# Kernel tuning notes

Measured on AMD Instinct MI355X. Metric: run time of the kernel, lower is better.

The kernel has to match this reference:

```python
import jax, jax.numpy as jnp
import numpy as np

H = 8          # num_heads
D = 64         # head_dim
IN = 512       # input_dim
SCALE = D ** -0.5


def setup_inputs() -> dict:
    key = jax.random.key(0)
    ks = jax.random.split(key, 5)
    b, n = 4, 2048
    inner = H * D
    x = jax.random.normal(ks[0], (b, n, IN), dtype=jnp.float32)
    # nn.Linear weights stored as [out, in]; apply as x @ W.T
    Wq = jax.random.normal(ks[1], (inner, IN), dtype=jnp.float32) * (IN ** -0.5)
    Wkv = jax.random.normal(ks[2], (2 * inner, IN), dtype=jnp.float32) * (IN ** -0.5)
    Wo = jax.random.normal(ks[3], (IN, inner), dtype=jnp.float32) * (inner ** -0.5)
    bo = jax.random.normal(ks[4], (IN,), dtype=jnp.float32) * 0.01
    return {"x": x, "Wq": Wq, "Wkv": Wkv, "Wo": Wo, "bo": bo}


def reference(x, Wq, Wkv, Wo, bo):
    b, n, _ = x.shape
    q = jnp.einsum('bni,oi->bno', x, Wq).reshape(b, n, H, D).transpose(0, 2, 1, 3)
    kv = jnp.einsum('bni,oi->bno', x, Wkv)
    k, v = jnp.split(kv, 2, axis=-1)
    k = k.reshape(b, n, H, D).transpose(0, 2, 1, 3)
    v = v.reshape(b, n, H, D).transpose(0, 2, 1, 3)
    attn = jax.nn.softmax(jnp.einsum('bhnd,bhmd->bhnm', q, k) * SCALE, axis=-1)
    # dropout in eval mode: identity
    out = jnp.einsum('bhnm,bhmd->bhnd', attn, v)
    out = out.transpose(0, 2, 1, 3).reshape(b, n, H * D)
    return jnp.einsum('bno,io->bni', out, Wo) + bo
```

## Files before the change

### kernel.cpp

```cpp
#include <hip/hip_runtime.h>
#include <hip/hip_bf16.h>

#define H_ 8
#define D_ 64
#define IN_ 512
#define B_ 4
#define N_ 2048
#define TOK_ (B_*N_)
#define CLOG2_ 0.18033688011112042f

typedef __attribute__((ext_vector_type(8))) short short8;
typedef __attribute__((ext_vector_type(4))) short bs4;
typedef __attribute__((ext_vector_type(4))) float f32x4;

__device__ __forceinline__ unsigned short f2bf(float f) {
  unsigned int u = __float_as_uint(f);
  u += 0x7FFFu + ((u >> 16) & 1u);
  return (unsigned short)(u >> 16);
}

__device__ __forceinline__ short8 cvt8(const float4 a, const float4 b) {
  union { short8 v; __hip_bfloat162 h[4]; } z;
  z.h[0] = __float22bfloat162_rn(make_float2(a.x, a.y));
  z.h[1] = __float22bfloat162_rn(make_float2(a.z, a.w));
  z.h[2] = __float22bfloat162_rn(make_float2(b.x, b.y));
  z.h[3] = __float22bfloat162_rn(make_float2(b.z, b.w));
  return z.v;
}

__device__ __forceinline__ bs4 pack4(float a, float b, float c, float d) {
  union { bs4 v; __hip_bfloat162 h[2]; } z;
  z.h[0] = __float22bfloat162_rn(make_float2(a, b));
  z.h[1] = __float22bfloat162_rn(make_float2(c, d));
  return z.v;
}

__device__ __forceinline__ short8 assemble_p(bs4 pa, bs4 pb) {
  union { bs4 v; unsigned int w[2]; } A, B;
  A.v = pa; B.v = pb;
  auto s0 = __builtin_amdgcn_permlane32_swap(A.w[0], B.w[0], false, false);
  auto s1 = __builtin_amdgcn_permlane32_swap(A.w[1], B.w[1], false, false);
  auto t0 = __builtin_amdgcn_permlane16_swap(s0[0], s0[1], false, false);
  auto t1 = __builtin_amdgcn_permlane16_swap(s1[0], s1[1], false, false);
  union { short8 v; unsigned int w[4]; } R;
  R.w[0] = t0[0];
  R.w[1] = t1[0];
  R.w[2] = t0[1];
  R.w[3] = t1[1];
  return R.v;
}

__device__ __forceinline__ void gld16(const unsigned short* g, unsigned short* l) {
  __builtin_amdgcn_global_load_lds(
      (const __attribute__((address_space(1))) void*)g,
      (__attribute__((address_space(3))) void*)l, 16, 0, 0);
}

__global__ __launch_bounds__(256) void conv_all_kernel(
    const float* __restrict__ x, const float* __restrict__ Wq,
    const float* __restrict__ Wkv, const float* __restrict__ Wo,
    unsigned short* __restrict__ xbf, unsigned short* __restrict__ wbf,
    unsigned short* __restrict__ wobf)
{
  const int b = blockIdx.x;
  const float* src;
  unsigned short* dst;
  size_t base;
  if (b < 2048)      { src = x;   dst = xbf;             base = (size_t)b * 2048; }
  else if (b < 2176) { src = Wq;  dst = wbf;             base = (size_t)(b - 2048) * 2048; }
  else if (b < 2432) { src = Wkv; dst = wbf + 512 * 512; base = (size_t)(b - 2176) * 2048; }
  else               { src = Wo;  dst = wobf;            base = (size_t)(b - 2432) * 2048; }
  size_t i = base + (size_t)threadIdx.x * 8;
  float4 a = *(const float4*)(src + i);
  float4 c = *(const float4*)(src + i + 4);
  *(short8*)(dst + i) = cvt8(a, c);
}

__global__ __launch_bounds__(256) void qkv_gemm_kernel(
    const unsigned short* __restrict__ xbf, const unsigned short* __restrict__ wbf,
    unsigned short* __restrict__ qws, unsigned short* __restrict__ kws,
    unsigned short* __restrict__ vws)
{
  __shared__ __attribute__((aligned(16))) unsigned short sm[128 * 136];

  const int lid = blockIdx.x + (blockIdx.y << 6);
  const int swz = (lid & 7) * 96 + (lid >> 3);
  const int t0 = (swz / 12) * 128;
  const int c0 = (swz % 12) * 128;
  const int cls = c0 >> 9;

  const int tid = threadIdx.x;
  const int wave = tid >> 6, lane = tid & 63;
  const int quad = lane >> 4, l16 = lane & 15;
  const int wm = wave >> 1, wn = wave & 1;

  const int r_ = tid >> 2;
  const int gc = (tid & 3) ^ (r_ & 3);
  const unsigned short* abase = xbf + (size_t)(t0 + r_) * IN_ + gc * 8;
  const unsigned short* bbase = wbf + (size_t)(c0 + r_) * IN_ + gc * 8;

  auto stage = [&](int k0, int buf) {
    unsigned short* sA = sm + buf * 8192;
    unsigned short* sB = sA + 4096;
    gld16(abase + k0,            sA + tid * 8);
    gld16(abase + 64 * IN_ + k0, sA + 2048 + tid * 8);
    gld16(bbase + k0,            sB + tid * 8);
    gld16(bbase + 64 * IN_ + k0, sB + 2048 + tid * 8);
  };

  f32x4 acc[4][4];
  #pragma unroll
  for (int i = 0; i < 4; i++)
    #pragma unroll
    for (int j = 0; j < 4; j++) acc[i][j] = (f32x4){0.f, 0.f, 0.f, 0.f};

  stage(0, 0);

  for (int kt = 0; kt < 16; kt++) {
    const int cur = kt & 1;
    __syncthreads();
    if (kt + 1 < 16) stage((kt + 1) * 32, cur ^ 1);
    const unsigned short* sA = sm + cur * 8192;
    const unsigned short* sB = sA + 4096;
    const int sw = ((quad ^ (l16 & 3)) << 3);
    short8 af[4], bf[4];
    #pragma unroll
    for (int mi = 0; mi < 4; mi++)
      af[mi] = *(const short8*)&sA[(wm * 64 + mi * 16 + l16) * 32 + sw];
    #pragma unroll
    for (int ni = 0; ni < 4; ni++)
      bf[ni] = *(const short8*)&sB[(wn * 64 + ni * 16 + l16) * 32 + sw];
    #pragma unroll
    for (int mi = 0; mi < 4; mi++)
      #pragma unroll
      for (int ni = 0; ni < 4; ni++)
        acc[mi][ni] = __builtin_amdgcn_mfma_f32_16x16x32_bf16(af[mi], bf[ni], acc[mi][ni], 0, 0, 0);
  }

  __syncthreads();

  if (cls < 2) {
    const float qs = (cls == 0) ? CLOG2_ : 1.0f;
    #pragma unroll
    for (int mi = 0; mi < 4; mi++) {
      const int row0 = wm * 64 + mi * 16 + quad * 4;
      #pragma unroll
      for (int ni = 0; ni < 4; ni++) {
        const int col = wn * 64 + ni * 16 + l16;
        #pragma unroll
        for (int r = 0; r < 4; r++)
          sm[(row0 + r) * 136 + col] = f2bf(acc[mi][ni][r] * qs);
      }
    }
    __syncthreads();
    const int row = tid >> 1, half = tid & 1;
    const int t = t0 + row, bb = t >> 11, nn = t & (N_ - 1);
    const int cw = (c0 & 511) + half * 64;
    const int hh = cw >> 6;
    unsigned short* dst = ((cls == 0) ? qws : kws) +
                          ((size_t)(bb * H_ + hh) * N_ + nn) * D_;
    const unsigned short* srcp = &sm[row * 136 + half * 64];
    #pragma unroll
    for (int j = 0; j < 8; j++)
      *(uint4*)(dst + j * 8) = *(const uint4*)(srcp + j * 8);
  } else {
    #pragma unroll
    for (int mi = 0; mi < 4; mi++) {
      const int tk = wm * 64 + mi * 16 + quad * 4;
      #pragma unroll
      for (int ni = 0; ni < 4; ni++) {
        const int col = wn * 64 + ni * 16 + l16;
        bs4 pk4 = pack4(acc[mi][ni][0], acc[mi][ni][1], acc[mi][ni][2], acc[mi][ni][3]);
        *(bs4*)&sm[col * 136 + tk] = pk4;
      }
    }
    __syncthreads();
    const int col = tid >> 1, half = tid & 1;
    const int cw = (c0 - 1024) + col;
    const int hh = cw >> 6, dd = cw & 63;
    const int bb = t0 >> 11, n0 = (t0 & (N_ - 1)) + half * 64;
    unsigned short* dst = vws + ((size_t)(bb * H_ + hh) * D_ + dd) * N_ + n0;
    const unsigned short* srcp = &sm[col * 136 + half * 64];
    #pragma unroll
    for (int j = 0; j < 8; j++)
      *(uint4*)(dst + j * 8) = *(const uint4*)(srcp + j * 8);
  }
}

__global__ __launch_bounds__(512, 4) void attention_kernel(
    const unsigned short* __restrict__ qws,
    const unsigned short* __restrict__ kws,
    const unsigned short* __restrict__ vws,
    unsigned short* __restrict__ ows)
{
  __shared__ __attribute__((aligned(16))) unsigned short sm[2][8192];
  __shared__ float sml[128];

  const int lid = blockIdx.x + (blockIdx.y << 4);
  const int swz = ((lid & 7) << 6) + (lid >> 3);
  const int q0 = (swz & 15) * 128;
  const int bh = swz >> 4;
  const int tid = threadIdx.x;
  const int wave = tid >> 6, lane = tid & 63;
  const int quad = lane >> 4, l16 = lane & 15;
  const int rbw = wave & 3;
  const int kh = wave >> 2;

  const unsigned short* qbase = qws + (size_t)bh * N_ * D_;
  const unsigned short* kbase = kws + (size_t)bh * N_ * D_;
  const unsigned short* vbase = vws + (size_t)bh * D_ * N_;

  short8 qf[2][2];
  #pragma unroll
  for (int rb = 0; rb < 2; rb++) {
    const int qrow = q0 + rbw * 32 + rb * 16 + l16;
    #pragma unroll
    for (int kc = 0; kc < 2; kc++)
      qf[rb][kc] = *(const short8*)(qbase + (size_t)qrow * D_ + kc * 32 + quad * 8);
  }

  f32x4 ot[2][4];
  f32x4 otl[2];
  #pragma unroll
  for (int rb = 0; rb < 2; rb++) {
    #pragma unroll
    for (int db = 0; db < 4; db++) ot[rb][db] = (f32x4){0.f, 0.f, 0.f, 0.f};
    otl[rb] = (f32x4){0.f, 0.f, 0.f, 0.f};
  }
  const short8 ones8 = {(short)0x3F80, (short)0x3F80, (short)0x3F80, (short)0x3F80,
                        (short)0x3F80, (short)0x3F80, (short)0x3F80, (short)0x3F80};

  const int r_ = tid >> 3;
  const int gc = (tid & 7) ^ (r_ & 7);
  const unsigned short* kst = kbase + (size_t)r_ * D_ + gc * 8;
  const unsigned short* vst = vbase + (size_t)r_ * N_ + gc * 8;

  {
    gld16(kst, &sm[0][0]    + tid * 8);
    gld16(vst, &sm[0][4096] + tid * 8);
  }

  for (int kt = 0; kt < N_ / 64; kt++) {
    const int cur = kt & 1;
    __syncthreads();
    if (kt + 1 < N_ / 64) {
      const int k0 = (kt + 1) * 64;
      gld16(kst + (size_t)k0 * D_, &sm[cur ^ 1][0]    + tid * 8);
      gld16(vst + k0,              &sm[cur ^ 1][4096] + tid * 8);
    }
    const unsigned short* Ks = &sm[cur][0];
    const unsigned short* Vs = &sm[cur][4096];

    f32x4 st[2][2];
    #pragma unroll
    for (int rb = 0; rb < 2; rb++)
      #pragma unroll
      for (int nb = 0; nb < 2; nb++) st[rb][nb] = (f32x4){0.f, 0.f, 0.f, 0.f};
    #pragma unroll
    for (int kc = 0; kc < 2; kc++) {
      const int sw = (((kc * 4 + quad) ^ (l16 & 7)) << 3);
      #pragma unroll
      for (int nb = 0; nb < 2; nb++) {
        short8 kf = *(const short8*)&Ks[(kh * 32 + nb * 16 + l16) * 64 + sw];
        st[0][nb] = __builtin_amdgcn_mfma_f32_16x16x32_bf16(kf, qf[0][kc], st[0][nb], 0, 0, 0);
        st[1][nb] = __builtin_amdgcn_mfma_f32_16x16x32_bf16(kf, qf[1][kc], st[1][nb], 0, 0, 0);
      }
    }

    short8 pA[2];
    #pragma unroll
    for (int rb = 0; rb < 2; rb++) {
      bs4 pf[2];
      #pragma unroll
      for (int nb = 0; nb < 2; nb++) {
        float p0 = __builtin_amdgcn_exp2f(st[rb][nb][0]);
        float p1 = __builtin_amdgcn_exp2f(st[rb][nb][1]);
        float p2 = __builtin_amdgcn_exp2f(st[rb][nb][2]);
        float p3 = __builtin_amdgcn_exp2f(st[rb][nb][3]);
        pf[nb] = pack4(p0, p1, p2, p3);
      }
      pA[rb] = assemble_p(pf[0], pf[1]);
    }

    {
      const int slot = (((kh * 4 + quad) ^ (l16 & 7)) << 3);
      short8 vf8[4];
      #pragma unroll
      for (int db = 0; db < 4; db++)
        vf8[db] = *(const short8*)&Vs[(db * 16 + l16) * 64 + slot];
      #pragma unroll
      for (int rb = 0; rb < 2; rb++) {
        #pragma unroll
        for (int db = 0; db < 4; db++)
          ot[rb][db] = __builtin_amdgcn_mfma_f32_16x16x32_bf16(vf8[db], pA[rb], ot[rb][db], 0, 0, 0);
        otl[rb] = __builtin_amdgcn_mfma_f32_16x16x32_bf16(ones8, pA[rb], otl[rb], 0, 0, 0);
      }
    }
  }

  __syncthreads();
  float* Of = (float*)sm;
  if (kh == 1) {
    #pragma unroll
    for (int rb = 0; rb < 2; rb++) {
      const int q = rbw * 32 + rb * 16 + l16;
      #pragma unroll
      for (int db = 0; db < 4; db++) {
        const int slot = (db * 4 + quad) ^ l16;
        *(f32x4*)&Of[q * 64 + slot * 4] = ot[rb][db];
      }
      if (quad == 0) sml[q] = otl[rb][0];
    }
  }
  __syncthreads();
  bs4 pk[2][4];
  if (kh == 0) {
    #pragma unroll
    for (int rb = 0; rb < 2; rb++) {
      const int q = rbw * 32 + rb * 16 + l16;
      const float inv = 1.f / (otl[rb][0] + sml[q]);
      #pragma unroll
      for (int db = 0; db < 4; db++) {
        const int slot = (db * 4 + quad) ^ l16;
        f32x4 p = *(const f32x4*)&Of[q * 64 + slot * 4];
        pk[rb][db] = pack4((ot[rb][db][0] + p[0]) * inv, (ot[rb][db][1] + p[1]) * inv,
                           (ot[rb][db][2] + p[2]) * inv, (ot[rb][db][3] + p[3]) * inv);
      }
    }
  }
  __syncthreads();
  unsigned short* Os = (unsigned short*)sm;
  if (kh == 0) {
    #pragma unroll
    for (int rb = 0; rb < 2; rb++)
      #pragma unroll
      for (int db = 0; db < 4; db++)
        *(bs4*)&Os[(rbw * 32 + rb * 16 + l16) * 72 + db * 16 + quad * 4] = pk[rb][db];
  }
  __syncthreads();
  const int b_ = bh >> 3, h_ = bh & 7;
  const int qloc = tid >> 2, chunk = tid & 3;
  unsigned short* dst = ows + ((size_t)b_ * N_ + q0 + qloc) * (H_ * D_) + h_ * 64 + chunk * 16;
  const unsigned short* srcp = &Os[qloc * 72 + chunk * 16];
  *(uint4*)dst = *(const uint4*)srcp;
  *(uint4*)(dst + 8) = *(const uint4*)(srcp + 8);
}

__global__ __launch_bounds__(256) void out_gemm_kernel(
    const unsigned short* __restrict__ ain, const unsigned short* __restrict__ wobf,
    const float* __restrict__ bo, float* __restrict__ y)
{
  __shared__ __attribute__((aligned(16))) unsigned short sm[12288];

  const int lid = blockIdx.x + (blockIdx.y << 6);
  const int swz = ((lid & 7) << 6) + (lid >> 3);
  const int t0 = (swz >> 3) * 128;
  const int c0 = (swz & 7) * 64;
  const int tid = threadIdx.x;
  const int wave = tid >> 6, lane = tid & 63;
  const int quad = lane >> 4, l16 = lane & 15;

  const int r_ = tid >> 2;
  const int gc = (tid & 3) ^ (r_ & 3);
  const unsigned short* abase = ain  + (size_t)(t0 + r_) * IN_ + gc * 8;
  const unsigned short* bbase = wobf + (size_t)(c0 + r_) * IN_ + gc * 8;

  auto stage = [&](int k0, int buf) {
    unsigned short* sA = sm + buf * 6144;
    unsigned short* sB = sA + 4096;
    gld16(abase + k0,            sA + tid * 8);
    gld16(abase + 64 * IN_ + k0, sA + 2048 + tid * 8);
    gld16(bbase + k0,            sB + tid * 8);
  };

  f32x4 acc[2][4];
  #pragma unroll
  for (int i = 0; i < 2; i++)
    #pragma unroll
    for (int j = 0; j < 4; j++) acc[i][j] = (f32x4){0.f, 0.f, 0.f, 0.f};

  stage(0, 0);

  for (int kt = 0; kt < 16; kt++) {
    const int cur = kt & 1;
    __syncthreads();
    if (kt + 1 < 16) stage((kt + 1) * 32, cur ^ 1);
    const unsigned short* sA = sm + cur * 6144;
    const unsigned short* sB = sA + 4096;
    const int sw = ((quad ^ (l16 & 3)) << 3);
    short8 af[2], bf[4];
    #pragma unroll
    for (int mi = 0; mi < 2; mi++)
      af[mi] = *(const short8*)&sA[(wave * 32 + mi * 16 + l16) * 32 + sw];
    #pragma unroll
    for (int ni = 0; ni < 4; ni++)
      bf[ni] = *(const short8*)&sB[(ni * 16 + l16) * 32 + sw];
    #pragma unroll
    for (int mi = 0; mi < 2; mi++)
      #pragma unroll
      for (int ni = 0; ni < 4; ni++)
        acc[mi][ni] = __builtin_amdgcn_mfma_f32_16x16x32_bf16(af[mi], bf[ni], acc[mi][ni], 0, 0, 0);
  }

  #pragma unroll
  for (int mi = 0; mi < 2; mi++) {
    const int t = t0 + wave * 32 + mi * 16 + quad * 4;
    #pragma unroll
    for (int ni = 0; ni < 4; ni++) {
      const int c = c0 + ni * 16 + l16;
      const float bias = bo[c];
      float* dst = y + (size_t)t * IN_ + c;
      dst[0]        = acc[mi][ni][0] + bias;
      dst[IN_]      = acc[mi][ni][1] + bias;
      dst[2 * IN_]  = acc[mi][ni][2] + bias;
      dst[3 * IN_]  = acc[mi][ni][3] + bias;
    }
  }
}

extern "C" void kernel_launch(void* const* d_in, const int* in_sizes, int n_in,
                              void* d_out, int out_size, void* d_ws, size_t ws_size,
                              hipStream_t stream) {
  const float* x   = (const float*)d_in[0];
  const float* Wq  = (const float*)d_in[1];
  const float* Wkv = (const float*)d_in[2];
  const float* Wo  = (const float*)d_in[3];
  const float* bo  = (const float*)d_in[4];
  float* out = (float*)d_out;

  unsigned short* qws  = (unsigned short*)d_ws;
  unsigned short* kws  = qws + (size_t)TOK_ * 512;
  unsigned short* vws  = kws + (size_t)TOK_ * 512;
  unsigned short* ows  = vws + (size_t)TOK_ * 512;
  unsigned short* wbf  = ows + (size_t)TOK_ * 512;
  unsigned short* wobf = wbf + (size_t)1536 * 512;
  unsigned short* xbf  = ows;

  conv_all_kernel<<<dim3(2560), 256, 0, stream>>>(x, Wq, Wkv, Wo, xbf, wbf, wobf);
  qkv_gemm_kernel<<<dim3(TOK_ / 128, 1536 / 128), 256, 0, stream>>>(xbf, wbf, qws, kws, vws);
  attention_kernel<<<dim3(N_ / 128, B_ * H_), 512, 0, stream>>>(qws, kws, vws, ows);
  out_gemm_kernel<<<dim3(TOK_ / 128, 512 / 64), 256, 0, stream>>>(ows, wobf, bo, out);
}
```

Baseline: 152.4 us.

## Fuse fp32-to-bf16 conversion into QKV and output GEMM loaders

Removes the separate conversion kernel and has the QKV GEMM load fp32 x and weights directly, converting to bf16 in registers before writing to LDS with a register-prefetch pipeline. The output GEMM likewise converts Wo on the fly while still using async LDS loads for the activation. This drops one launch and the bf16 staging round-trip through memory. In exchange, the QKV GEMM reads twice the bytes per tile (fp32), and each x tile is re-read and re-converted by all 12 column blocks. It also loses the direct global-to-LDS loads.

Measured after the change: 153.5 us. About the same (+0.7%).

```diff
diff --git a/kernel.cpp b/kernel.cpp
--- a/kernel.cpp
+++ b/kernel.cpp
@@ -56,28 +56,9 @@
       (__attribute__((address_space(3))) void*)l, 16, 0, 0);
 }
 
-__global__ __launch_bounds__(256) void conv_all_kernel(
+__global__ __launch_bounds__(256) void qkv_gemm_kernel(
     const float* __restrict__ x, const float* __restrict__ Wq,
-    const float* __restrict__ Wkv, const float* __restrict__ Wo,
-    unsigned short* __restrict__ xbf, unsigned short* __restrict__ wbf,
-    unsigned short* __restrict__ wobf)
-{
-  const int b = blockIdx.x;
-  const float* src;
-  unsigned short* dst;
-  size_t base;
-  if (b < 2048)      { src = x;   dst = xbf;             base = (size_t)b * 2048; }
-  else if (b < 2176) { src = Wq;  dst = wbf;             base = (size_t)(b - 2048) * 2048; }
-  else if (b < 2432) { src = Wkv; dst = wbf + 512 * 512; base = (size_t)(b - 2176) * 2048; }
-  else               { src = Wo;  dst = wobf;            base = (size_t)(b - 2432) * 2048; }
-  size_t i = base + (size_t)threadIdx.x * 8;
-  float4 a = *(const float4*)(src + i);
-  float4 c = *(const float4*)(src + i + 4);
-  *(short8*)(dst + i) = cvt8(a, c);
-}
-
-__global__ __launch_bounds__(256) void qkv_gemm_kernel(
-    const unsigned short* __restrict__ xbf, const unsigned short* __restrict__ wbf,
+    const float* __restrict__ Wkv,
     unsigned short* __restrict__ qws, unsigned short* __restrict__ kws,
     unsigned short* __restrict__ vws)
 {
@@ -96,16 +77,29 @@
 
   const int r_ = tid >> 2;
   const int gc = (tid & 3) ^ (r_ & 3);
-  const unsigned short* abase = xbf + (size_t)(t0 + r_) * IN_ + gc * 8;
-  const unsigned short* bbase = wbf + (size_t)(c0 + r_) * IN_ + gc * 8;
-
-  auto stage = [&](int k0, int buf) {
+  const float* asrc = x + (size_t)(t0 + r_) * IN_ + gc * 8;
+  const float* bsrc = ((c0 < 512) ? Wq + (size_t)c0 * IN_
+                                  : Wkv + (size_t)(c0 - 512) * IN_)
+                      + (size_t)r_ * IN_ + gc * 8;
+
+  float4 ra[4], rb[4];
+  auto load = [&](int k0) {
+    ra[0] = *(const float4*)(asrc + k0);
+    ra[1] = *(const float4*)(asrc + k0 + 4);
+    ra[2] = *(const float4*)(asrc + 64 * IN_ + k0);
+    ra[3] = *(const float4*)(asrc + 64 * IN_ + k0 + 4);
+    rb[0] = *(const float4*)(bsrc + k0);
+    rb[1] = *(const float4*)(bsrc + k0 + 4);
+    rb[2] = *(const float4*)(bsrc + 64 * IN_ + k0);
+    rb[3] = *(const float4*)(bsrc + 64 * IN_ + k0 + 4);
+  };
+  auto write = [&](int buf) {
     unsigned short* sA = sm + buf * 8192;
     unsigned short* sB = sA + 4096;
-    gld16(abase + k0,            sA + tid * 8);
-    gld16(abase + 64 * IN_ + k0, sA + 2048 + tid * 8);
-    gld16(bbase + k0,            sB + tid * 8);
-    gld16(bbase + 64 * IN_ + k0, sB + 2048 + tid * 8);
+    *(short8*)(sA + tid * 8)        = cvt8(ra[0], ra[1]);
+    *(short8*)(sA + 2048 + tid * 8) = cvt8(ra[2], ra[3]);
+    *(short8*)(sB + tid * 8)        = cvt8(rb[0], rb[1]);
+    *(short8*)(sB + 2048 + tid * 8) = cvt8(rb[2], rb[3]);
   };
 
   f32x4 acc[4][4];
@@ -114,13 +108,15 @@
     #pragma unroll
     for (int j = 0; j < 4; j++) acc[i][j] = (f32x4){0.f, 0.f, 0.f, 0.f};
 
-  stage(0, 0);
+  load(0); write(0); load(32);
 
   for (int kt = 0; kt < 16; kt++) {
-    const int cur = kt & 1;
     __syncthreads();
-    if (kt + 1 < 16) stage((kt + 1) * 32, cur ^ 1);
-    const unsigned short* sA = sm + cur * 8192;
+    if (kt + 1 < 16) {
+      write((kt + 1) & 1);
+      if (kt + 2 < 16) load((kt + 2) * 32);
+    }
+    const unsigned short* sA = sm + (kt & 1) * 8192;
     const unsigned short* sB = sA + 4096;
     const int sw = ((quad ^ (l16 & 3)) << 3);
     short8 af[4], bf[4];
@@ -347,7 +343,7 @@
 }
 
 __global__ __launch_bounds__(256) void out_gemm_kernel(
-    const unsigned short* __restrict__ ain, const unsigned short* __restrict__ wobf,
+    const unsigned short* __restrict__ ain, const float* __restrict__ Wo,
     const float* __restrict__ bo, float* __restrict__ y)
 {
   __shared__ __attribute__((aligned(16))) unsigned short sm[12288];
@@ -362,15 +358,21 @@
 
   const int r_ = tid >> 2;
   const int gc = (tid & 3) ^ (r_ & 3);
-  const unsigned short* abase = ain  + (size_t)(t0 + r_) * IN_ + gc * 8;
-  const unsigned short* bbase = wobf + (size_t)(c0 + r_) * IN_ + gc * 8;
-
-  auto stage = [&](int k0, int buf) {
+  const unsigned short* abase = ain + (size_t)(t0 + r_) * IN_ + gc * 8;
+  const float* bsrc = Wo + (size_t)(c0 + r_) * IN_ + gc * 8;
+
+  float4 rb[2];
+  auto loadB = [&](int k0) {
+    rb[0] = *(const float4*)(bsrc + k0);
+    rb[1] = *(const float4*)(bsrc + k0 + 4);
+  };
+  auto writeB = [&](int buf) {
+    *(short8*)(sm + buf * 6144 + 4096 + tid * 8) = cvt8(rb[0], rb[1]);
+  };
+  auto stageA = [&](int k0, int buf) {
     unsigned short* sA = sm + buf * 6144;
-    unsigned short* sB = sA + 4096;
     gld16(abase + k0,            sA + tid * 8);
     gld16(abase + 64 * IN_ + k0, sA + 2048 + tid * 8);
-    gld16(bbase + k0,            sB + tid * 8);
   };
 
   f32x4 acc[2][4];
@@ -379,13 +381,16 @@
     #pragma unroll
     for (int j = 0; j < 4; j++) acc[i][j] = (f32x4){0.f, 0.f, 0.f, 0.f};
 
-  stage(0, 0);
+  loadB(0); writeB(0); stageA(0, 0); loadB(32);
 
   for (int kt = 0; kt < 16; kt++) {
-    const int cur = kt & 1;
     __syncthreads();
-    if (kt + 1 < 16) stage((kt + 1) * 32, cur ^ 1);
-    const unsigned short* sA = sm + cur * 6144;
+    if (kt + 1 < 16) {
+      writeB((kt + 1) & 1);
+      stageA((kt + 1) * 32, (kt + 1) & 1);
+      if (kt + 2 < 16) loadB((kt + 2) * 32);
+    }
+    const unsigned short* sA = sm + (kt & 1) * 6144;
     const unsigned short* sB = sA + 4096;
     const int sw = ((quad ^ (l16 & 3)) << 3);
     short8 af[2], bf[4];
@@ -432,12 +437,8 @@
   unsigned short* kws  = qws + (size_t)TOK_ * 512;
   unsigned short* vws  = kws + (size_t)TOK_ * 512;
   unsigned short* ows  = vws + (size_t)TOK_ * 512;
-  unsigned short* wbf  = ows + (size_t)TOK_ * 512;
-  unsigned short* wobf = wbf + (size_t)1536 * 512;
-  unsigned short* xbf  = ows;
-
-  conv_all_kernel<<<dim3(2560), 256, 0, stream>>>(x, Wq, Wkv, Wo, xbf, wbf, wobf);
-  qkv_gemm_kernel<<<dim3(TOK_ / 128, 1536 / 128), 256, 0, stream>>>(xbf, wbf, qws, kws, vws);
+
+  qkv_gemm_kernel<<<dim3(TOK_ / 128, 1536 / 128), 256, 0, stream>>>(x, Wq, Wkv, qws, kws, vws);
   attention_kernel<<<dim3(N_ / 128, B_ * H_), 512, 0, stream>>>(qws, kws, vws, ows);
-  out_gemm_kernel<<<dim3(TOK_ / 128, 512 / 64), 256, 0, stream>>>(ows, wobf, bo, out);
-}
+  out_gemm_kernel<<<dim3(TOK_ / 128, 512 / 64), 256, 0, stream>>>(ows, Wo, bo, out);
+}
```
